# Kernel tuning notes

Measured on AMD Instinct MI355X. Metric: run time of the kernel, lower is better.

The kernel has to match this reference:

```python
import jax, jax.numpy as jnp
import numpy as np

B, T, C = 4, 2048, 1024


def setup_inputs() -> dict:
    key = jax.random.key(0)
    ks = jax.random.split(key, 5)
    s = 1.0 / np.sqrt(C)
    return {
        "X": jax.random.normal(ks[0], (B, T, C), dtype=jnp.float32),
        "Wq": jax.random.normal(ks[1], (C, C), dtype=jnp.float32) * s,
        "Wk": jax.random.normal(ks[2], (C, C), dtype=jnp.float32) * s,
        "Wv": jax.random.normal(ks[3], (C, C), dtype=jnp.float32) * s,
        "Wo": jax.random.normal(ks[4], (C, C), dtype=jnp.float32) * s,
    }


def reference(X, Wq, Wk, Wv, Wo):
    Bx, Tx, Cx = X.shape
    Q = X @ Wq  # [B,T,C]
    K = X @ Wk
    V = X @ Wv
    scores = jnp.einsum('btc,bsc->bts', Q, K) / jnp.sqrt(jnp.asarray(Cx, X.dtype))
    # causal mask: position t attends to s <= t
    causal = jnp.tril(jnp.ones((Tx, Tx), dtype=bool))
    scores = jnp.where(causal, scores, jnp.asarray(-jnp.inf, scores.dtype))
    weights = jax.nn.softmax(scores, axis=-1)
    out = jnp.einsum('bts,bsc->btc', weights, V)
    return out @ Wo
```

## Files before the change

### kernel.cpp

```cpp
#include <hip/hip_runtime.h>
#include <hip/hip_bf16.h>
#include <cmath>


typedef __attribute__((ext_vector_type(8))) __bf16 bf16x8;
typedef __attribute__((ext_vector_type(8))) short short8;
typedef __attribute__((ext_vector_type(4))) float f32x4;

__device__ __forceinline__ unsigned short f2bf(float f) {
  union { float f; unsigned u; } v; v.f = f;
  unsigned u = v.u;
  u += ((u >> 16) & 1u) + 0x7fffu;
  return (unsigned short)(u >> 16);
}
__device__ __forceinline__ float bf2f(unsigned short h) {
  union { unsigned u; float f; } v; v.u = ((unsigned)h) << 16;
  return v.f;
}

#define GLDS(gp, sp)                                                           \
  __builtin_amdgcn_global_load_lds(                                            \
      (const __attribute__((address_space(1))) void*)(gp),                     \
      (__attribute__((address_space(3))) void*)(sp), 16, 0, 0)

__global__ void prep(const float* __restrict__ X,
                     const float* __restrict__ w0, const float* __restrict__ w1,
                     const float* __restrict__ w2, const float* __restrict__ w3,
                     unsigned short* __restrict__ Xb,
                     unsigned short* __restrict__ wcat,
                     unsigned short* __restrict__ wvb,
                     unsigned short* __restrict__ wot,
                     int n) {
  if (blockIdx.z == 2) {
    int bx = blockIdx.x * 32, by = blockIdx.y * 32;
    int tx = threadIdx.x, ty = threadIdx.y;
#pragma unroll
    for (int i = 0; i < 32; i += 8) {
      size_t idx = (size_t)(by + ty + i) * n + bx + tx;
      wvb[idx] = f2bf(w2[idx]);
    }
  } else if (blockIdx.z < 4) {
    const float* src = blockIdx.z == 0 ? w0 : blockIdx.z == 1 ? w1 : w3;
    unsigned short* dst = blockIdx.z == 0 ? wcat
                          : blockIdx.z == 1 ? wcat + (size_t)n * n : wot;
    __shared__ float tile[32][33];
    int bx = blockIdx.x * 32, by = blockIdx.y * 32;
    int tx = threadIdx.x, ty = threadIdx.y;
#pragma unroll
    for (int i = 0; i < 32; i += 8)
      tile[ty + i][tx] = src[(size_t)(by + ty + i) * n + bx + tx];
    __syncthreads();
#pragma unroll
    for (int i = 0; i < 32; i += 8)
      dst[(size_t)(bx + ty + i) * n + by + tx] = f2bf(tile[tx][ty + i]);
  } else {
    const int bid = (blockIdx.z - 4) * 1024 + blockIdx.y * 32 + blockIdx.x;
    const int t = threadIdx.y * 32 + threadIdx.x;
    const int i = (bid * 256 + t) * 4;
    float4 f = *(const float4*)(X + i);
    ushort4 o = make_ushort4(f2bf(f.x), f2bf(f.y), f2bf(f.z), f2bf(f.w));
    *(ushort4*)(Xb + i) = o;
  }
}

template <typename OutT, int NW>
__global__ __launch_bounds__(NW * 64, NW / 2)
void gemm_bt(const unsigned short* __restrict__ A, int lda, long long sA,
             const unsigned short* __restrict__ B, int ldb, long long sB,
             OutT* __restrict__ Cp, int ldc, long long sC,
             int K, float alpha, int tri, int kcap, int gx) {
  A  += (long long)blockIdx.z * sA;
  B  += (long long)blockIdx.z * sB;
  Cp += (long long)blockIdx.z * sC;

  int by, bx;
  if (tri) {
    int idx = blockIdx.x;
    idx = (idx & 7) * ((int)gridDim.x >> 3) + (idx >> 3);
    by = (int)((sqrtf(8.f * idx + 1.f) - 1.f) * 0.5f);
    while (by * (by + 1) / 2 > idx) --by;
    while ((by + 1) * (by + 2) / 2 <= idx) ++by;
    bx = idx - by * (by + 1) / 2;
  } else if (gx > 0) {
    const int id = blockIdx.x;
    const int gs = gx * 8;
    const int g = id / gs, r = id - g * gs;
    bx = r >> 3;
    by = g * 8 + (r & 7);
    if (kcap) by = (gridDim.x / gx) - 1 - by;
  } else {
    by = blockIdx.y;
    bx = blockIdx.x;
  }
  const int m0 = by * 128;
  const int n0 = bx * 128;
  const int Keff = kcap ? min(K, m0 + 128) : K;

  const int tid  = threadIdx.x;
  const int lane = tid & 63;
  const int w    = tid >> 6;
  const int wm   = (NW == 4) ? (w >> 1) * 64 : (w >> 1) * 32;
  const int wn   = (w & 1) * 64;
  const int quad = lane >> 4;
  const int l16  = lane & 15;
  constexpr int AI = (NW == 4) ? 4 : 2;
  constexpr int NR = 128 / (NW * 8);

  __shared__ unsigned short As[8192];
  __shared__ unsigned short Bs[8192];

  f32x4 acc[AI][4];
#pragma unroll
  for (int i = 0; i < AI; ++i)
#pragma unroll
    for (int j = 0; j < 4; ++j)
      acc[i][j] = (f32x4){0.f, 0.f, 0.f, 0.f};

  const int srow = tid >> 3;
  const int scol = ((tid & 7) ^ (srow & 7)) * 8;
  const unsigned short* gA = A + (long long)(m0 + srow) * lda + scol;
  const unsigned short* gB = B + (long long)(n0 + srow) * ldb + scol;
  const int rsw = l16 & 7;

  for (int kt = 0; kt < Keff; kt += 64) {
    __syncthreads();
#pragma unroll
    for (int r = 0; r < NR; ++r) {
      GLDS(gA + (long long)(r * NW * 8) * lda + kt, As + r * NW * 512 + tid * 8);
      GLDS(gB + (long long)(r * NW * 8) * ldb + kt, Bs + r * NW * 512 + tid * 8);
    }
    __syncthreads();
#pragma unroll
    for (int ks = 0; ks < 2; ++ks) {
      bf16x8 af[AI], bfr[4];
#pragma unroll
      for (int i = 0; i < AI; ++i)
        af[i] = *(const bf16x8*)(As + (wm + i * 16 + l16) * 64 +
                                 ((ks * 4 + quad) ^ rsw) * 8);
#pragma unroll
      for (int j = 0; j < 4; ++j)
        bfr[j] = *(const bf16x8*)(Bs + (wn + j * 16 + l16) * 64 +
                                  ((ks * 4 + quad) ^ rsw) * 8);
#pragma unroll
      for (int i = 0; i < AI; ++i)
#pragma unroll
        for (int j = 0; j < 4; ++j)
          acc[i][j] = __builtin_amdgcn_mfma_f32_16x16x32_bf16(af[i], bfr[j],
                                                              acc[i][j], 0, 0, 0);
    }
  }

#pragma unroll
  for (int i = 0; i < AI; ++i) {
#pragma unroll
    for (int j = 0; j < 4; ++j) {
      const int row = m0 + wm + i * 16 + quad * 4;
      const int col = n0 + wn + j * 16 + l16;
#pragma unroll
      for (int r = 0; r < 4; ++r) {
        float v = acc[i][j][r] * alpha;
        if constexpr (sizeof(OutT) == 2)
          Cp[(long long)(row + r) * ldc + col] = (OutT)f2bf(v);
        else
          Cp[(long long)(row + r) * ldc + col] = v;
      }
    }
  }
}

__global__ __launch_bounds__(256, 2)
void gemm_qkv(const unsigned short* __restrict__ A, int lda,
              const unsigned short* __restrict__ B, int ldb,
              unsigned short* __restrict__ Cp, int K, int gx) {
  const int id = blockIdx.x;
  const int gs = gx * 8;
  const int g = id / gs, r = id - g * gs;
  const int bx = r >> 3;
  const int by = g * 8 + (r & 7);
  const int m0 = by * 128;
  const int n0 = bx * 128;

  const int tid  = threadIdx.x;
  const int lane = tid & 63;
  const int w    = tid >> 6;
  const int wm   = (w >> 1) * 64;
  const int wn   = (w & 1) * 64;
  const int quad = lane >> 4;
  const int l16  = lane & 15;

  __shared__ unsigned short As[8192];
  __shared__ unsigned short Bs[8192];

  f32x4 acc[4][4];
#pragma unroll
  for (int i = 0; i < 4; ++i)
#pragma unroll
    for (int j = 0; j < 4; ++j)
      acc[i][j] = (f32x4){0.f, 0.f, 0.f, 0.f};

  const int srow = tid >> 3;
  const int scol = ((tid & 7) ^ (srow & 7)) * 8;
  const unsigned short* gA = A + (long long)(m0 + srow) * lda + scol;
  const unsigned short* gB = B + (long long)(n0 + srow) * ldb + scol;
  const int rsw = l16 & 7;

  for (int kt = 0; kt < K; kt += 64) {
    __syncthreads();
#pragma unroll
    for (int r2 = 0; r2 < 4; ++r2) {
      GLDS(gA + (long long)(r2 * 32) * lda + kt, As + r2 * 2048 + tid * 8);
      GLDS(gB + (long long)(r2 * 32) * ldb + kt, Bs + r2 * 2048 + tid * 8);
    }
    __syncthreads();
#pragma unroll
    for (int ks = 0; ks < 2; ++ks) {
      bf16x8 af[4], bfr[4];
#pragma unroll
      for (int i = 0; i < 4; ++i)
        af[i] = *(const bf16x8*)(As + (wm + i * 16 + l16) * 64 +
                                 ((ks * 4 + quad) ^ rsw) * 8);
#pragma unroll
      for (int j = 0; j < 4; ++j)
        bfr[j] = *(const bf16x8*)(Bs + (wn + j * 16 + l16) * 64 +
                                  ((ks * 4 + quad) ^ rsw) * 8);
#pragma unroll
      for (int i = 0; i < 4; ++i)
#pragma unroll
        for (int j = 0; j < 4; ++j)
          acc[i][j] = __builtin_amdgcn_mfma_f32_16x16x32_bf16(af[i], bfr[j],
                                                              acc[i][j], 0, 0, 0);
    }
  }

#pragma unroll
  for (int i = 0; i < 4; ++i) {
#pragma unroll
    for (int j = 0; j < 4; ++j) {
      const int row = m0 + wm + i * 16 + quad * 4;
      const int col = n0 + wn + j * 16 + l16;
      if (col >= 2048) {
        const int b = row >> 11, t = row & 2047, cv = col - 2048;
        ushort4 o = make_ushort4(f2bf(acc[i][j][0]), f2bf(acc[i][j][1]),
                                 f2bf(acc[i][j][2]), f2bf(acc[i][j][3]));
        *(ushort4*)(Cp + 16777216LL + ((long long)(b * 1024 + cv)) * 2048 + t) = o;
      } else {
        unsigned short* dst = Cp + (col >= 1024 ? 8388608LL - 1024 : 0);
#pragma unroll
        for (int r2 = 0; r2 < 4; ++r2)
          dst[(long long)(row + r2) * 1024 + col] = f2bf(acc[i][j][r2]);
      }
    }
  }
}

__global__ __launch_bounds__(256)
void softmax_causal(const unsigned short* __restrict__ Sin,
                    unsigned short* __restrict__ Sout, int T) {
  const long long row = blockIdx.x;
  const int t = (int)(row & (long long)(T - 1));
  const int limit = ((t >> 7) + 1) << 7;
  const unsigned short* pin = Sin + row * T;
  unsigned short* pout = Sout + row * T;
  const int tid  = threadIdx.x;
  const int base = tid * 8;
  const bool active = base < limit;

  short8 raw = {};
  if (active) raw = *(const short8*)(pin + base);
  float x[8];
  float mx = -1e30f;
#pragma unroll
  for (int j = 0; j < 8; ++j) {
    bool valid = active && (base + j) <= t;
    x[j] = valid ? bf2f((unsigned short)raw[j]) : -1e30f;
    mx = fmaxf(mx, x[j]);
  }
#pragma unroll
  for (int off = 32; off > 0; off >>= 1) mx = fmaxf(mx, __shfl_xor(mx, off));
  __shared__ float red[8];
  const int wv = tid >> 6;
  if ((tid & 63) == 0) red[wv] = mx;
  __syncthreads();
  mx = fmaxf(fmaxf(red[0], red[1]), fmaxf(red[2], red[3]));

  float sum = 0.f;
#pragma unroll
  for (int j = 0; j < 8; ++j) {
    bool valid = active && (base + j) <= t;
    x[j] = valid ? __expf(x[j] - mx) : 0.f;
    sum += x[j];
  }
#pragma unroll
  for (int off = 32; off > 0; off >>= 1) sum += __shfl_xor(sum, off);
  if ((tid & 63) == 0) red[4 + wv] = sum;
  __syncthreads();
  sum = red[4] + red[5] + red[6] + red[7];
  const float inv = 1.f / sum;

  if (active) {
    unsigned short out[8];
#pragma unroll
    for (int j = 0; j < 8; ++j) out[j] = f2bf(x[j] * inv);
    *(short8*)(pout + base) = *(const short8*)out;
  }
}

extern "C" void kernel_launch(void* const* d_in, const int* in_sizes, int n_in,
                              void* d_out, int out_size, void* d_ws,
                              size_t ws_size, hipStream_t stream) {
  (void)in_sizes; (void)n_in; (void)out_size; (void)ws_size;
  const int Bb = 4, T = 2048, C = 1024;
  const int M = Bb * T;

  const float* X  = (const float*)d_in[0];
  const float* Wq = (const float*)d_in[1];
  const float* Wk = (const float*)d_in[2];
  const float* Wv = (const float*)d_in[3];
  const float* Wo = (const float*)d_in[4];

  char* w = (char*)d_ws;
  unsigned short* Wcat = (unsigned short*)w; w += (size_t)3 * C * C * 2;
  unsigned short* Q    = (unsigned short*)w; w += (size_t)M * C * 2;
  unsigned short* Kb   = (unsigned short*)w; w += (size_t)M * C * 2;
  unsigned short* Vt   = (unsigned short*)w; w += (size_t)M * C * 2;
  unsigned short* Xb   = (unsigned short*)w; w += (size_t)M * C * 2;
  (void)Kb;
  unsigned short* Wvb  = (unsigned short*)d_out;
  unsigned short* Wot  = (unsigned short*)d_out + (size_t)C * C;
  unsigned short* S    = (unsigned short*)d_out;
  unsigned short* Sn   = Q;

  prep<<<dim3(32, 32, 12), dim3(32, 8), 0, stream>>>(X, Wq, Wk, Wv, Wo, Xb,
                                                     Wcat, Wvb, Wot, C);

  gemm_bt<unsigned short, 4><<<dim3(C / 128, C / 128, 1), dim3(256), 0, stream>>>(
      Wot, C, 0, Wvb, C, 0, Wcat + (size_t)2 * C * C, C, 0, C, 1.f, 0, 0, 0);

  gemm_qkv<<<dim3((3 * C / 128) * (M / 128)), dim3(256), 0, stream>>>(
      Xb, C, Wcat, C, Q, C, 3 * C / 128);

  const int ntri = (T / 128) * (T / 128 + 1) / 2;
  gemm_bt<unsigned short, 8><<<dim3(ntri, 1, Bb), dim3(512), 0, stream>>>(
      Q, C, (long long)T * C, Kb, C, (long long)T * C,
      S, T, (long long)T * T, C, 0.03125f, 1, 0, 0);

  softmax_causal<<<M, 256, 0, stream>>>(S, Sn, T);

  gemm_bt<float, 8><<<dim3((C / 128) * (T / 128), 1, Bb), dim3(512), 0, stream>>>(
      Sn, T, (long long)T * T, Vt, T, (long long)C * T,
      (float*)d_out, C, (long long)T * C, T, 1.f, 0, 1, C / 128);
}
```

Measured before the change: 244.1 us.

## Fuse causal softmax into QK^T epilogue and normalize in PV GEMM epilogue

Drops the separate softmax kernel. The QK^T GEMM epilogue now computes exp of the scaled scores without subtracting a row max, zeroes masked entries, writes bf16 probabilities and atomically adds row sums into a float buffer. The PV GEMM epilogue divides by those row sums. This saves one full read and write pass over the T×T score matrix, at the cost of atomics, an extra memset and possible overflow risk because the max-subtraction is gone, which only holds for bounded score ranges.

New measurement: 248.4 us. About the same (+1.8%).

```diff
diff --git a/kernel.cpp b/kernel.cpp
--- a/kernel.cpp
+++ b/kernel.cpp
@@ -68,10 +68,12 @@
 void gemm_bt(const unsigned short* __restrict__ A, int lda, long long sA,
              const unsigned short* __restrict__ B, int ldb, long long sB,
              OutT* __restrict__ Cp, int ldc, long long sC,
-             int K, float alpha, int tri, int kcap, int gx) {
+             int K, float alpha, int tri, int kcap, int gx,
+             float* __restrict__ rsum, long long sR, int mode) {
   A  += (long long)blockIdx.z * sA;
   B  += (long long)blockIdx.z * sB;
   Cp += (long long)blockIdx.z * sC;
+  if (mode != 0) rsum += (long long)blockIdx.z * sR;
 
   int by, bx;
   if (tri) {
@@ -150,6 +152,55 @@
     }
   }
 
+  if constexpr (sizeof(OutT) == 2) {
+    if (mode == 1) {
+#pragma unroll
+      for (int i = 0; i < AI; ++i) {
+        const int row = m0 + wm + i * 16 + quad * 4;
+        float rs[4] = {0.f, 0.f, 0.f, 0.f};
+#pragma unroll
+        for (int j = 0; j < 4; ++j) {
+          const int col = n0 + wn + j * 16 + l16;
+#pragma unroll
+          for (int r = 0; r < 4; ++r) {
+            float e = __expf(acc[i][j][r] * alpha);
+            if (col > row + r) e = 0.f;
+            unsigned short h = f2bf(e);
+            Cp[(long long)(row + r) * ldc + col] = (OutT)h;
+            rs[r] += bf2f(h);
+          }
+        }
+#pragma unroll
+        for (int m = 8; m; m >>= 1)
+#pragma unroll
+          for (int r = 0; r < 4; ++r) rs[r] += __shfl_xor(rs[r], m);
+        if (l16 == 0) {
+#pragma unroll
+          for (int r = 0; r < 4; ++r) atomicAdd(&rsum[row + r], rs[r]);
+        }
+      }
+      return;
+    }
+  }
+  if constexpr (sizeof(OutT) == 4) {
+    if (mode == 2) {
+#pragma unroll
+      for (int i = 0; i < AI; ++i) {
+        const int row = m0 + wm + i * 16 + quad * 4;
+        float inv[4];
+#pragma unroll
+        for (int r = 0; r < 4; ++r) inv[r] = 1.f / rsum[row + r];
+#pragma unroll
+        for (int j = 0; j < 4; ++j) {
+          const int col = n0 + wn + j * 16 + l16;
+#pragma unroll
+          for (int r = 0; r < 4; ++r)
+            Cp[(long long)(row + r) * ldc + col] = acc[i][j][r] * inv[r];
+        }
+      }
+      return;
+    }
+  }
 #pragma unroll
   for (int i = 0; i < AI; ++i) {
 #pragma unroll
@@ -171,7 +222,8 @@
 __global__ __launch_bounds__(256, 2)
 void gemm_qkv(const unsigned short* __restrict__ A, int lda,
               const unsigned short* __restrict__ B, int ldb,
-              unsigned short* __restrict__ Cp, int K, int gx) {
+              unsigned short* __restrict__ Cqk,
+              unsigned short* __restrict__ Cvt, int K, int gx) {
   const int id = blockIdx.x;
   const int gs = gx * 8;
   const int g = id / gs, r = id - g * gs;
@@ -242,66 +294,14 @@
         const int b = row >> 11, t = row & 2047, cv = col - 2048;
         ushort4 o = make_ushort4(f2bf(acc[i][j][0]), f2bf(acc[i][j][1]),
                                  f2bf(acc[i][j][2]), f2bf(acc[i][j][3]));
-        *(ushort4*)(Cp + 16777216LL + ((long long)(b * 1024 + cv)) * 2048 + t) = o;
+        *(ushort4*)(Cvt + ((long long)(b * 1024 + cv)) * 2048 + t) = o;
       } else {
-        unsigned short* dst = Cp + (col >= 1024 ? 8388608LL - 1024 : 0);
+        unsigned short* dst = Cqk + (col >= 1024 ? 8388608LL - 1024 : 0);
 #pragma unroll
         for (int r2 = 0; r2 < 4; ++r2)
           dst[(long long)(row + r2) * 1024 + col] = f2bf(acc[i][j][r2]);
       }
     }
-  }
-}
-
-__global__ __launch_bounds__(256)
-void softmax_causal(const unsigned short* __restrict__ Sin,
-                    unsigned short* __restrict__ Sout, int T) {
-  const long long row = blockIdx.x;
-  const int t = (int)(row & (long long)(T - 1));
-  const int limit = ((t >> 7) + 1) << 7;
-  const unsigned short* pin = Sin + row * T;
-  unsigned short* pout = Sout + row * T;
-  const int tid  = threadIdx.x;
-  const int base = tid * 8;
-  const bool active = base < limit;
-
-  short8 raw = {};
-  if (active) raw = *(const short8*)(pin + base);
-  float x[8];
-  float mx = -1e30f;
-#pragma unroll
-  for (int j = 0; j < 8; ++j) {
-    bool valid = active && (base + j) <= t;
-    x[j] = valid ? bf2f((unsigned short)raw[j]) : -1e30f;
-    mx = fmaxf(mx, x[j]);
-  }
-#pragma unroll
-  for (int off = 32; off > 0; off >>= 1) mx = fmaxf(mx, __shfl_xor(mx, off));
-  __shared__ float red[8];
-  const int wv = tid >> 6;
-  if ((tid & 63) == 0) red[wv] = mx;
-  __syncthreads();
-  mx = fmaxf(fmaxf(red[0], red[1]), fmaxf(red[2], red[3]));
-
-  float sum = 0.f;
-#pragma unroll
-  for (int j = 0; j < 8; ++j) {
-    bool valid = active && (base + j) <= t;
-    x[j] = valid ? __expf(x[j] - mx) : 0.f;
-    sum += x[j];
-  }
-#pragma unroll
-  for (int off = 32; off > 0; off >>= 1) sum += __shfl_xor(sum, off);
-  if ((tid & 63) == 0) red[4 + wv] = sum;
-  __syncthreads();
-  sum = red[4] + red[5] + red[6] + red[7];
-  const float inv = 1.f / sum;
-
-  if (active) {
-    unsigned short out[8];
-#pragma unroll
-    for (int j = 0; j < 8; ++j) out[j] = f2bf(x[j] * inv);
-    *(short8*)(pout + base) = *(const short8*)out;
   }
 }
 
@@ -320,33 +320,34 @@
 
   char* w = (char*)d_ws;
   unsigned short* Wcat = (unsigned short*)w; w += (size_t)3 * C * C * 2;
-  unsigned short* Q    = (unsigned short*)w; w += (size_t)M * C * 2;
-  unsigned short* Kb   = (unsigned short*)w; w += (size_t)M * C * 2;
+  unsigned short* Pp   = (unsigned short*)w; w += (size_t)M * T * 2;
   unsigned short* Vt   = (unsigned short*)w; w += (size_t)M * C * 2;
   unsigned short* Xb   = (unsigned short*)w; w += (size_t)M * C * 2;
-  (void)Kb;
-  unsigned short* Wvb  = (unsigned short*)d_out;
-  unsigned short* Wot  = (unsigned short*)d_out + (size_t)C * C;
-  unsigned short* S    = (unsigned short*)d_out;
-  unsigned short* Sn   = Q;
+  float*          Rs   = (float*)w;          w += (size_t)M * 4;
+  unsigned short* Wvb = (unsigned short*)d_out;
+  unsigned short* Wot = (unsigned short*)d_out + (size_t)C * C;
+  unsigned short* Qd  = (unsigned short*)d_out;
+  unsigned short* Kd  = Qd + (size_t)M * C;
+
+  hipMemsetAsync(Rs, 0, (size_t)M * sizeof(float), stream);
 
   prep<<<dim3(32, 32, 12), dim3(32, 8), 0, stream>>>(X, Wq, Wk, Wv, Wo, Xb,
                                                      Wcat, Wvb, Wot, C);
 
   gemm_bt<unsigned short, 4><<<dim3(C / 128, C / 128, 1), dim3(256), 0, stream>>>(
-      Wot, C, 0, Wvb, C, 0, Wcat + (size_t)2 * C * C, C, 0, C, 1.f, 0, 0, 0);
+      Wot, C, 0, Wvb, C, 0, Wcat + (size_t)2 * C * C, C, 0, C, 1.f, 0, 0, 0,
+      nullptr, 0, 0);
 
   gemm_qkv<<<dim3((3 * C / 128) * (M / 128)), dim3(256), 0, stream>>>(
-      Xb, C, Wcat, C, Q, C, 3 * C / 128);
+      Xb, C, Wcat, C, Qd, Vt, C, 3 * C / 128);
 
   const int ntri = (T / 128) * (T / 128 + 1) / 2;
   gemm_bt<unsigned short, 8><<<dim3(ntri, 1, Bb), dim3(512), 0, stream>>>(
-      Q, C, (long long)T * C, Kb, C, (long long)T * C,
-      S, T, (long long)T * T, C, 0.03125f, 1, 0, 0);
-
-  softmax_causal<<<M, 256, 0, stream>>>(S, Sn, T);
+      Qd, C, (long long)T * C, Kd, C, (long long)T * C,
+      Pp, T, (long long)T * T, C, 0.03125f, 1, 0, 0, Rs, T, 1);
 
   gemm_bt<float, 8><<<dim3((C / 128) * (T / 128), 1, Bb), dim3(512), 0, stream>>>(
-      Sn, T, (long long)T * T, Vt, T, (long long)C * T,
-      (float*)d_out, C, (long long)T * C, T, 1.f, 0, 1, C / 128);
-}
+      Pp, T, (long long)T * T, Vt, T, (long long)C * T,
+      (float*)d_out, C, (long long)T * C, T, 1.f, 0, 1, C / 128,
+      Rs, T, 2);
+}
```
